# Kernel optimization log

Hardware: AMD Instinct MI355X
Metric: run time of the kernel (lower is better)

## Reference

```python
import jax, jax.numpy as jnp
import numpy as np

S, D, H = 2048, 2048, 16
HD = D // H  # head dim = 128
LN_EPS = 1e-5


def _ln(x, g, b):
    mu = jnp.mean(x, axis=-1, keepdims=True)
    var = jnp.var(x, axis=-1, keepdims=True)
    return (x - mu) / jnp.sqrt(var + LN_EPS) * g + b


def setup_inputs() -> dict:
    key = jax.random.key(0)
    ks = jax.random.split(key, 8)
    B = 2
    s = 0.02  # weight init scale
    return {
        "x": jax.random.normal(ks[0], (B, S, D), jnp.float32),
        "Wq": jax.random.normal(ks[1], (D, D), jnp.float32) * s,
        "bq": jnp.zeros((D,), jnp.float32),
        "Wk": jax.random.normal(ks[2], (D, D), jnp.float32) * s,
        "bk": jnp.zeros((D,), jnp.float32),
        "Wv": jax.random.normal(ks[3], (D, D), jnp.float32) * s,
        "bv": jnp.zeros((D,), jnp.float32),
        "Wo": jax.random.normal(ks[4], (D, D), jnp.float32) * s,
        "bo": jnp.zeros((D,), jnp.float32),
        "ln1_g": jnp.ones((D,), jnp.float32),
        "ln1_b": jnp.zeros((D,), jnp.float32),
        "ln2_g": jnp.ones((D,), jnp.float32),
        "ln2_b": jnp.zeros((D,), jnp.float32),
        "W1": jax.random.normal(ks[5], (4 * D, D), jnp.float32) * s,
        "b1": jnp.zeros((4 * D,), jnp.float32),
        "W2": jax.random.normal(ks[6], (D, 4 * D), jnp.float32) * s,
        "b2": jnp.zeros((D,), jnp.float32),
    }


def reference(x, Wq, bq, Wk, bk, Wv, bv, Wo, bo,
              ln1_g, ln1_b, ln2_g, ln2_b, W1, b1, W2, b2):
    causal = jnp.tril(jnp.ones((S, S), bool))  # [S, S] lower-triangular mask
    neg = jnp.finfo(x.dtype).min
    inv_sqrt_hd = 1.0 / jnp.sqrt(jnp.asarray(HD, x.dtype))

    def block(xs):  # xs: [S, D] (equinox module is per-sequence; vmapped over batch)
        h = _ln(xs, ln1_g, ln1_b)
        q = (h @ Wq.T + bq).reshape(S, H, HD)
        k = (h @ Wk.T + bk).reshape(S, H, HD)
        v = (h @ Wv.T + bv).reshape(S, H, HD)
        logits = jnp.einsum('shd,Shd->hsS', q, k) * inv_sqrt_hd
        logits = jnp.where(causal, logits, neg)
        attn = jax.nn.softmax(logits, axis=-1)
        o = jnp.einsum('hsS,Shd->shd', attn, v).reshape(S, D)
        h = h + (o @ Wo.T + bo)          # residual of post-ln1 value (as in source)
        h2 = _ln(h, ln2_g, ln2_b)
        m = jax.nn.gelu(h2 @ W1.T + b1) @ W2.T + b2
        return h2 + m                    # residual of post-ln2 value (as in source)

    return jax.vmap(block)(x)
```

## Files before the change

kernel.cpp:

```cpp
#include <hip/hip_runtime.h>
#include <hip/hip_bf16.h>
#include <math.h>

#define DD   2048
#define SS   2048
#define HH   16
#define HDIM 128
#define BB   2
#define MM   4096
#define D4   8192

using bf16x8 = __attribute__((ext_vector_type(8))) short;
using f32x4  = __attribute__((ext_vector_type(4))) float;
using f32x16 = __attribute__((ext_vector_type(16))) float;

__device__ __forceinline__ ushort f2bf(float x) {
  uint u = __builtin_bit_cast(uint, x);
  u += 0x7FFFu + ((u >> 16) & 1u);
  return (ushort)(u >> 16);
}
__device__ __forceinline__ float bf2f(ushort u) {
  return __builtin_bit_cast(float, (uint)u << 16);
}
__device__ __forceinline__ uint pkbf2(float a, float b) {
  return (uint)f2bf(a) | ((uint)f2bf(b) << 16);
}

__device__ __forceinline__ float gelu_f(float v) {
  float u = 0.7978845608028654f * (v + 0.044715f * v * v * v);
  float e = __expf(2.0f * u);
  float th = 1.0f - 2.0f / (e + 1.0f);
  return 0.5f * v * (1.0f + th);
}

__device__ __forceinline__ void gload_lds16(const void* g, void* l) {
  __builtin_amdgcn_global_load_lds(
      (const __attribute__((address_space(1))) void*)g,
      (__attribute__((address_space(3))) void*)l, 16, 0, 0);
}

__global__ __launch_bounds__(256) void cvt_f32_bf16(
    const float* __restrict__ in, ushort* __restrict__ out, int n4) {
  int i = blockIdx.x * 256 + threadIdx.x;
  if (i >= n4) return;
  float4 v = ((const float4*)in)[i];
  ushort4 o;
  o.x = f2bf(v.x); o.y = f2bf(v.y); o.z = f2bf(v.z); o.w = f2bf(v.w);
  ((ushort4*)out)[i] = o;
}

__global__ __launch_bounds__(256) void ln_rows(
    const float* __restrict__ in, const float* __restrict__ gam,
    const float* __restrict__ bet, ushort* __restrict__ outb) {
  int row = blockIdx.x;
  int t = threadIdx.x;
  const float4* r4 = (const float4*)(in + (size_t)row * DD);
  float4 v0 = r4[t], v1 = r4[t + 256];
  float s = v0.x + v0.y + v0.z + v0.w + v1.x + v1.y + v1.z + v1.w;
  __shared__ float redA[4], redB[4];
  #pragma unroll
  for (int off = 32; off >= 1; off >>= 1) s += __shfl_xor(s, off);
  if ((t & 63) == 0) redA[t >> 6] = s;
  __syncthreads();
  float mean = (redA[0] + redA[1] + redA[2] + redA[3]) * (1.0f / DD);
  float d0 = v0.x - mean, d1 = v0.y - mean, d2 = v0.z - mean, d3 = v0.w - mean;
  float d4 = v1.x - mean, d5 = v1.y - mean, d6 = v1.z - mean, d7 = v1.w - mean;
  float q = d0*d0 + d1*d1 + d2*d2 + d3*d3 + d4*d4 + d5*d5 + d6*d6 + d7*d7;
  #pragma unroll
  for (int off = 32; off >= 1; off >>= 1) q += __shfl_xor(q, off);
  if ((t & 63) == 0) redB[t >> 6] = q;
  __syncthreads();
  float var = (redB[0] + redB[1] + redB[2] + redB[3]) * (1.0f / DD);
  float rstd = rsqrtf(var + 1e-5f);
  const float4* g4 = (const float4*)gam;
  const float4* b4 = (const float4*)bet;
  float4 g0 = g4[t], g1 = g4[t + 256], bb0 = b4[t], bb1 = b4[t + 256];
  float4 y0, y1;
  y0.x = d0 * rstd * g0.x + bb0.x;  y0.y = d1 * rstd * g0.y + bb0.y;
  y0.z = d2 * rstd * g0.z + bb0.z;  y0.w = d3 * rstd * g0.w + bb0.w;
  y1.x = d4 * rstd * g1.x + bb1.x;  y1.y = d5 * rstd * g1.y + bb1.y;
  y1.z = d6 * rstd * g1.z + bb1.z;  y1.w = d7 * rstd * g1.w + bb1.w;
  ushort4 u0, u1;
  u0.x = f2bf(y0.x); u0.y = f2bf(y0.y); u0.z = f2bf(y0.z); u0.w = f2bf(y0.w);
  u1.x = f2bf(y1.x); u1.y = f2bf(y1.y); u1.z = f2bf(y1.z); u1.w = f2bf(y1.w);
  ushort4* ob4 = (ushort4*)(outb + (size_t)row * DD);
  ob4[t] = u0; ob4[t + 256] = u1;
}

template <int OMODE, bool GELU_, bool RES_>
__global__ __launch_bounds__(512, 2) void gemm2(
    const ushort* __restrict__ A, const ushort* __restrict__ Bt,
    const float* __restrict__ pb0, const float* __restrict__ pb1,
    const float* __restrict__ pb2, const ushort* __restrict__ res,
    void* __restrict__ Cout, int M, int N, int K) {
  extern __shared__ __align__(16) ushort smem[];
  const int nbm = M >> 8, nbn = N >> 7;
  const int nwg = nbm * nbn;
  int wg = blockIdx.x;
  int wg2 = (wg & 7) * (nwg >> 3) + (wg >> 3);
  int bm = wg2 % nbm, bn = wg2 / nbm;
  int m0 = bm << 8, n0 = bn << 7;
  int t = threadIdx.x, lane = t & 63, w = t >> 6;
  int wm = w >> 2, wn = w & 3;
  int lr = lane & 15, lg = lane >> 4;

  auto stage = [&](int kt, int slot) {
    int k0 = kt << 6;
    ushort* lA = smem + slot * 24576;
    ushort* lB = lA + 16384;
    #pragma unroll
    for (int r = 0; r < 4; r++) {
      int idx = (r << 9) + t;
      int row = idx >> 3, ch = idx & 7;
      gload_lds16(A + (size_t)(m0 + row) * K + k0 + ((ch ^ (row & 7)) << 3),
                  lA + idx * 8);
    }
    #pragma unroll
    for (int r = 0; r < 2; r++) {
      int idx = (r << 9) + t;
      int row = idx >> 3, ch = idx & 7;
      gload_lds16(Bt + (size_t)(n0 + row) * K + k0 + ((ch ^ (row & 7)) << 3),
                  lB + idx * 8);
    }
  };

  f32x4 acc[8][2] = {};
  const int NT = K >> 6;
  stage(0, 0);
  stage(1, 1);
  int slot = 0;
  for (int kt = 0; kt < NT; ++kt) {
    __builtin_amdgcn_sched_barrier(0);
    if (kt + 1 < NT)
      asm volatile("s_waitcnt vmcnt(6) lgkmcnt(0)" ::: "memory");
    else
      asm volatile("s_waitcnt vmcnt(0) lgkmcnt(0)" ::: "memory");
    __builtin_amdgcn_s_barrier();
    __builtin_amdgcn_sched_barrier(0);
    if (kt + 2 < NT) {
      int s2 = slot + 2; if (s2 >= 3) s2 -= 3;
      stage(kt + 2, s2);
    }
    const ushort* lA = smem + slot * 24576;
    const ushort* lB = lA + 16384;
    bf16x8 af[8][2], bfr[2][2];
    #pragma unroll
    for (int mi = 0; mi < 8; mi++) {
      int row = wm * 128 + mi * 16 + lr;
      #pragma unroll
      for (int ks = 0; ks < 2; ks++)
        af[mi][ks] = *(const bf16x8*)
            &lA[row * 64 + (((ks * 4 + lg) ^ (row & 7)) << 3)];
    }
    #pragma unroll
    for (int ni = 0; ni < 2; ni++) {
      int row = wn * 32 + ni * 16 + lr;
      #pragma unroll
      for (int ks = 0; ks < 2; ks++)
        bfr[ni][ks] = *(const bf16x8*)
            &lB[row * 64 + (((ks * 4 + lg) ^ (row & 7)) << 3)];
    }
    __builtin_amdgcn_s_setprio(1);
    #pragma unroll
    for (int ks = 0; ks < 2; ks++)
      #pragma unroll
      for (int mi = 0; mi < 8; mi++)
        #pragma unroll
        for (int ni = 0; ni < 2; ni++)
          acc[mi][ni] = __builtin_amdgcn_mfma_f32_16x16x32_bf16(
              af[mi][ks], bfr[ni][ks], acc[mi][ni], 0, 0, 0);
    __builtin_amdgcn_s_setprio(0);
    slot = (slot + 1 == 3) ? 0 : slot + 1;
  }

  if (OMODE == 3) {
    int seg = n0 >> 11;
    const float* pb = (seg == 0) ? pb0 : (seg == 1) ? pb1 : pb2;
    int c0 = n0 & 2047;
    float bv[2];
    #pragma unroll
    for (int ni = 0; ni < 2; ni++) bv[ni] = pb[c0 + wn * 32 + ni * 16 + lr];
    if (seg < 2) {
      ushort* q_or_k = (ushort*)Cout + (size_t)seg * MM * DD;
      #pragma unroll
      for (int mi = 0; mi < 8; mi++) {
        #pragma unroll
        for (int r = 0; r < 4; r++) {
          int m = m0 + wm * 128 + mi * 16 + lg * 4 + r;
          #pragma unroll
          for (int ni = 0; ni < 2; ni++) {
            int col = c0 + wn * 32 + ni * 16 + lr;
            q_or_k[(size_t)m * DD + col] = f2bf(acc[mi][ni][r] + bv[ni]);
          }
        }
      }
    } else {
      ushort* vT = (ushort*)Cout + (size_t)2 * MM * DD;
      #pragma unroll
      for (int mi = 0; mi < 8; mi++) {
        int mg = m0 + wm * 128 + mi * 16 + lg * 4;
        int bb_ = mg >> 11, sb = mg & 2047;
        #pragma unroll
        for (int ni = 0; ni < 2; ni++) {
          int col = c0 + wn * 32 + ni * 16 + lr;
          int h = col >> 7, d = col & 127;
          ushort4 u4;
          u4.x = f2bf(acc[mi][ni][0] + bv[ni]);
          u4.y = f2bf(acc[mi][ni][1] + bv[ni]);
          u4.z = f2bf(acc[mi][ni][2] + bv[ni]);
          u4.w = f2bf(acc[mi][ni][3] + bv[ni]);
          size_t idx = ((size_t)(bb_ * 16 + h) * 128 + d) * 2048 + sb;
          *(ushort4*)&vT[idx] = u4;
        }
      }
    }
    return;
  }

  float bv[2];
  #pragma unroll
  for (int ni = 0; ni < 2; ni++) bv[ni] = pb0[n0 + wn * 32 + ni * 16 + lr];
  #pragma unroll
  for (int mi = 0; mi < 8; mi++) {
    #pragma unroll
    for (int r = 0; r < 4; r++) {
      int m = m0 + wm * 128 + mi * 16 + lg * 4 + r;
      #pragma unroll
      for (int ni = 0; ni < 2; ni++) {
        int n = n0 + wn * 32 + ni * 16 + lr;
        size_t idx = (size_t)m * N + n;
        float v = acc[mi][ni][r] + bv[ni];
        if (RES_) v += bf2f(res[idx]);
        if (GELU_) v = gelu_f(v);
        if (OMODE == 1) ((ushort*)Cout)[idx] = f2bf(v);
        else            ((float*)Cout)[idx] = v;
      }
    }
  }
}

__global__ __launch_bounds__(256) void attn_fwd(
    const ushort* __restrict__ qb, const ushort* __restrict__ kb,
    const ushort* __restrict__ vTb, ushort* __restrict__ ob) {
  extern __shared__ __align__(16) ushort asm_[];
  ushort* KsB = asm_;
  ushort* VsB = asm_ + 16384;
  ushort* Pw  = asm_ + 32768 + (threadIdx.x >> 6) * 2048;

  int blk = blockIdx.x;
  int i15 = blk & 15;
  int qt = (blk & 256) ? i15 : 15 - i15;
  int bh = blk >> 4;
  int b = bh >> 4, h = bh & 15;
  int q0 = qt << 7;
  int t = threadIdx.x, lane = t & 63, w = t >> 6;
  int l31 = lane & 31, hi = lane >> 5;
  const size_t base = (size_t)b * SS * DD + (size_t)h * HDIM;
  const ushort* qp = qb + base;
  const ushort* kp = kb + base;
  const ushort* vp = vTb + (size_t)bh * HDIM * SS;
  int wq0 = q0 + w * 32;
  int qg = wq0 + l31;

  bf16x8 qf[8];
  #pragma unroll
  for (int kk = 0; kk < 8; kk++)
    qf[kk] = *(const bf16x8*)(qp + (size_t)qg * DD + kk * 16 + hi * 8);

  auto stageKV = [&](int it, int buf) {
    int kv0 = it * 64;
    ushort* Kd = KsB + buf * 8192;
    ushort* Vd = VsB + buf * 8192;
    #pragma unroll
    for (int ii = 0; ii < 4; ii++) {
      int chunk = ii * 256 + t;
      int row = chunk >> 4, cc = chunk & 15;
      gload_lds16(kp + (size_t)(kv0 + row) * DD + ((cc ^ (row & 15)) << 3),
                  Kd + chunk * 8);
    }
    #pragma unroll
    for (int ii = 0; ii < 4; ii++) {
      int chunk = ii * 256 + t;
      int row = chunk >> 3, cc = chunk & 7;
      gload_lds16(vp + (size_t)row * SS + kv0 + ((cc ^ (row & 7)) << 3),
                  Vd + chunk * 8);
    }
  };

  f32x16 o[4] = {};
  float mu = -1e30f, lrow = 0.f;
  const float csc = 0.08838834764831845f * 1.4426950408889634f;

  int nIter = 2 * qt + 2;
  stageKV(0, 0);
  asm volatile("s_waitcnt vmcnt(0)" ::: "memory");
  __builtin_amdgcn_s_barrier();
  int cur = 0;
  for (int it = 0; it < nIter; ++it) {
    int kv0 = it * 64;
    if (it + 1 < nIter) stageKV(it + 1, cur ^ 1);

    if (kv0 <= wq0 + 31) {
      const ushort* Kc = KsB + cur * 8192;
      const ushort* Vc = VsB + cur * 8192;
      f32x16 s2[2] = {};
      #pragma unroll
      for (int nt = 0; nt < 2; nt++) {
        int row = nt * 32 + l31;
        #pragma unroll
        for (int kk = 0; kk < 8; kk++) {
          bf16x8 kf = *(const bf16x8*)
              &Kc[row * 128 + (((kk * 2 + hi) ^ (row & 15)) << 3)];
          s2[nt] = __builtin_amdgcn_mfma_f32_32x32x16_bf16(kf, qf[kk], s2[nt],
                                                           0, 0, 0);
        }
      }
      bool full = (kv0 + 63 <= wq0);
      float pm[4] = {-3e38f, -3e38f, -3e38f, -3e38f};
      if (full) {
        #pragma unroll
        for (int nt = 0; nt < 2; nt++)
          #pragma unroll
          for (int g2 = 0; g2 < 4; g2++)
            #pragma unroll
            for (int i = 0; i < 4; i++) {
              float u = s2[nt][g2 * 4 + i] * csc;
              s2[nt][g2 * 4 + i] = u;
              pm[i] = fmaxf(pm[i], u);
            }
      } else {
        #pragma unroll
        for (int nt = 0; nt < 2; nt++)
          #pragma unroll
          for (int g2 = 0; g2 < 4; g2++)
            #pragma unroll
            for (int i = 0; i < 4; i++) {
              int kvl = nt * 32 + g2 * 8 + 4 * hi + i;
              float u = (kv0 + kvl > qg) ? -3e38f : s2[nt][g2 * 4 + i] * csc;
              s2[nt][g2 * 4 + i] = u;
              pm[i] = fmaxf(pm[i], u);
            }
      }
      float mx = fmaxf(fmaxf(pm[0], pm[1]), fmaxf(pm[2], pm[3]));
      mx = fmaxf(mx, __shfl_xor(mx, 32));
      if (!__all(mx - mu <= 8.0f)) {
        float mnew = fmaxf(mu, mx);
        float fr = exp2f(mu - mnew);
        mu = mnew;
        lrow *= fr;
        #pragma unroll
        for (int dt = 0; dt < 4; dt++)
          #pragma unroll
          for (int r = 0; r < 16; r++) o[dt][r] *= fr;
      }
      float ps[4] = {0.f, 0.f, 0.f, 0.f};
      #pragma unroll
      for (int nt = 0; nt < 2; nt++)
        #pragma unroll
        for (int g2 = 0; g2 < 4; g2++)
          #pragma unroll
          for (int i = 0; i < 4; i++) {
            float p = exp2f(s2[nt][g2 * 4 + i] - mu);
            s2[nt][g2 * 4 + i] = p;
            ps[i] += p;
          }
      float sum = (ps[0] + ps[1]) + (ps[2] + ps[3]);
      sum += __shfl_xor(sum, 32);
      lrow += sum;
      #pragma unroll
      for (int nt = 0; nt < 2; nt++) {
        #pragma unroll
        for (int g2 = 0; g2 < 4; g2++) {
          uint2 u;
          u.x = pkbf2(s2[nt][g2 * 4 + 0], s2[nt][g2 * 4 + 1]);
          u.y = pkbf2(s2[nt][g2 * 4 + 2], s2[nt][g2 * 4 + 3]);
          int cp = (nt * 4 + g2) ^ (l31 & 7);
          *(uint2*)&Pw[l31 * 64 + cp * 8 + hi * 4] = u;
        }
      }
      asm volatile("s_waitcnt lgkmcnt(0)" ::: "memory");
      #pragma unroll
      for (int kk = 0; kk < 4; kk++) {
        bf16x8 pf = *(const bf16x8*)
            &Pw[l31 * 64 + (((kk * 2 + hi) ^ (l31 & 7)) << 3)];
        #pragma unroll
        for (int dt = 0; dt < 4; dt++) {
          int drow = dt * 32 + l31;
          bf16x8 vf = *(const bf16x8*)
              &Vc[drow * 64 + (((kk * 2 + hi) ^ (drow & 7)) << 3)];
          o[dt] = __builtin_amdgcn_mfma_f32_32x32x16_bf16(vf, pf, o[dt],
                                                          0, 0, 0);
        }
      }
    }
    asm volatile("s_waitcnt vmcnt(0)" ::: "memory");
    __builtin_amdgcn_s_barrier();
    cur ^= 1;
  }

  float inv = 1.0f / lrow;
  #pragma unroll
  for (int dt = 0; dt < 4; dt++) {
    #pragma unroll
    for (int g2 = 0; g2 < 4; g2++) {
      uint2 u;
      u.x = pkbf2(o[dt][g2 * 4 + 0] * inv, o[dt][g2 * 4 + 1] * inv);
      u.y = pkbf2(o[dt][g2 * 4 + 2] * inv, o[dt][g2 * 4 + 3] * inv);
      int d = dt * 32 + 8 * g2 + 4 * hi;
      *(uint2*)&ob[base + (size_t)qg * DD + d] = u;
    }
  }
}

extern "C" void kernel_launch(void* const* d_in, const int* in_sizes, int n_in,
                              void* d_out, int out_size, void* d_ws,
                              size_t ws_size, hipStream_t stream) {
  const float* x    = (const float*)d_in[0];
  const float* Wq   = (const float*)d_in[1];
  const float* bq   = (const float*)d_in[2];
  const float* Wk   = (const float*)d_in[3];
  const float* bk   = (const float*)d_in[4];
  const float* Wv   = (const float*)d_in[5];
  const float* bv   = (const float*)d_in[6];
  const float* Wo   = (const float*)d_in[7];
  const float* bo   = (const float*)d_in[8];
  const float* ln1g = (const float*)d_in[9];
  const float* ln1b = (const float*)d_in[10];
  const float* ln2g = (const float*)d_in[11];
  const float* ln2b = (const float*)d_in[12];
  const float* W1   = (const float*)d_in[13];
  const float* b1   = (const float*)d_in[14];
  const float* W2   = (const float*)d_in[15];
  const float* b2   = (const float*)d_in[16];

  char* ws = (char*)d_ws;
  ushort* Wqkvb = (ushort*)(ws);
  ushort* Wob   = Wqkvb + (size_t)3 * DD * DD;
  ushort* W1b = (ushort*)(ws);
  ushort* W2b = W1b + (size_t)D4 * DD;
  ushort* qkvb = (ushort*)(ws + 67108864);
  ushort* qbf = qkvb;
  ushort* kbf = qbf + (size_t)MM * DD;
  ushort* vTt = kbf + (size_t)MM * DD;
  ushort* aob = vTt + (size_t)MM * DD;
  ushort* gb  = (ushort*)(ws + 67108864);
  ushort* hb  = (ushort*)(ws + 167772160);
  ushort* h2b = hb;
  float* h2in = (float*)(ws + 184549376);
  float* out  = (float*)d_out;

  const int LDSB = 147456;
  const int LDSA = 81920;
  (void)hipFuncSetAttribute((const void*)gemm2<3, false, false>,
                      hipFuncAttributeMaxDynamicSharedMemorySize, LDSB);
  (void)hipFuncSetAttribute((const void*)gemm2<0, false, true>,
                      hipFuncAttributeMaxDynamicSharedMemorySize, LDSB);
  (void)hipFuncSetAttribute((const void*)gemm2<1, true, false>,
                      hipFuncAttributeMaxDynamicSharedMemorySize, LDSB);
  (void)hipFuncSetAttribute((const void*)attn_fwd,
                      hipFuncAttributeMaxDynamicSharedMemorySize, LDSA);

  dim3 blk(256);
  dim3 gblk(512);
  cvt_f32_bf16<<<DD * DD / 1024, blk, 0, stream>>>(Wq, Wqkvb, DD * DD / 4);
  cvt_f32_bf16<<<DD * DD / 1024, blk, 0, stream>>>(Wk, Wqkvb + (size_t)DD * DD, DD * DD / 4);
  cvt_f32_bf16<<<DD * DD / 1024, blk, 0, stream>>>(Wv, Wqkvb + (size_t)2 * DD * DD, DD * DD / 4);
  cvt_f32_bf16<<<DD * DD / 1024, blk, 0, stream>>>(Wo, Wob, DD * DD / 4);
  ln_rows<<<MM, blk, 0, stream>>>(x, ln1g, ln1b, hb);
  gemm2<3, false, false><<<768, gblk, LDSB, stream>>>(
      hb, Wqkvb, bq, bk, bv, nullptr, qkvb, MM, 3 * DD, DD);
  attn_fwd<<<512, blk, LDSA, stream>>>(qbf, kbf, vTt, aob);
  gemm2<0, false, true><<<256, gblk, LDSB, stream>>>(
      aob, Wob, bo, bo, bo, hb, h2in, MM, DD, DD);
  ln_rows<<<MM, blk, 0, stream>>>(h2in, ln2g, ln2b, h2b);
  cvt_f32_bf16<<<D4 * DD / 1024, blk, 0, stream>>>(W1, W1b, D4 * DD / 4);
  cvt_f32_bf16<<<D4 * DD / 1024, blk, 0, stream>>>(W2, W2b, D4 * DD / 4);
  gemm2<1, true, false><<<1024, gblk, LDSB, stream>>>(
      h2b, W1b, b1, b1, b1, nullptr, gb, MM, D4, DD);
  gemm2<0, false, true><<<256, gblk, LDSB, stream>>>(
      gb, W2b, b2, b2, b2, h2b, out, MM, DD, D4);
}
```

Before: 628.7 us.

## Add 256x256 quadrant-pipelined GEMM kernel and split-K for MLP down projection

Adds a new GEMM kernel with 256x256 tiles, double-buffered direct global-to-LDS loads, and a quadrant-by-quadrant MFMA schedule that overlaps the next k-tile's loads with compute. It replaces the QKV and MLP-up GEMMs. The W2 GEMM becomes split-K over two halves writing bf16 partials, and a new elementwise kernel sums them with the bias and residual. This should raise per-tile data reuse and fill the GPU better on the K=8192 GEMM. The cost is an extra partial-sum pass over memory and bf16 rounding of the partials.

```diff
diff --git a/kernel.cpp b/kernel.cpp
--- a/kernel.cpp
+++ b/kernel.cpp
@@ -90,8 +90,7 @@
 template <int OMODE, bool GELU_, bool RES_>
 __global__ __launch_bounds__(512, 2) void gemm2(
     const ushort* __restrict__ A, const ushort* __restrict__ Bt,
-    const float* __restrict__ pb0, const float* __restrict__ pb1,
-    const float* __restrict__ pb2, const ushort* __restrict__ res,
+    const float* __restrict__ pb0, const ushort* __restrict__ res,
     void* __restrict__ Cout, int M, int N, int K) {
   extern __shared__ __align__(16) ushort smem[];
   const int nbm = M >> 8, nbn = N >> 7;
@@ -173,13 +172,191 @@
     slot = (slot + 1 == 3) ? 0 : slot + 1;
   }
 
-  if (OMODE == 3) {
+  float bv[2];
+  #pragma unroll
+  for (int ni = 0; ni < 2; ni++) bv[ni] = pb0[n0 + wn * 32 + ni * 16 + lr];
+  #pragma unroll
+  for (int mi = 0; mi < 8; mi++) {
+    #pragma unroll
+    for (int r = 0; r < 4; r++) {
+      int m = m0 + wm * 128 + mi * 16 + lg * 4 + r;
+      #pragma unroll
+      for (int ni = 0; ni < 2; ni++) {
+        int n = n0 + wn * 32 + ni * 16 + lr;
+        size_t idx = (size_t)m * N + n;
+        float v = acc[mi][ni][r] + bv[ni];
+        if (RES_) v += bf2f(res[idx]);
+        if (GELU_) v = gelu_f(v);
+        if (OMODE == 1) ((ushort*)Cout)[idx] = f2bf(v);
+        else            ((float*)Cout)[idx] = v;
+      }
+    }
+  }
+}
+
+#define MF16(MQ, NQ, BARR) \
+  { _Pragma("unroll") for (int ks = 0; ks < 2; ks++) { \
+    _Pragma("unroll") for (int fm = 0; fm < 4; fm++) { \
+      _Pragma("unroll") for (int fn = 0; fn < 2; fn++) { \
+        acc[MQ * 4 + fm][NQ * 2 + fn] = \
+            __builtin_amdgcn_mfma_f32_16x16x32_bf16( \
+                aR[fm][ks], BARR[fn][ks], acc[MQ * 4 + fm][NQ * 2 + fn], \
+                0, 0, 0); } } } }
+
+template <int OMODE, bool GELU_>
+__global__ __launch_bounds__(512, 2) void gemm8(
+    const ushort* __restrict__ A, const ushort* __restrict__ Bt,
+    const float* __restrict__ pb0, const float* __restrict__ pb1,
+    const float* __restrict__ pb2,
+    void* __restrict__ Cout, int M, int N, int Kfull, int Kloc) {
+  extern __shared__ __align__(16) ushort smem[];
+  const int nbm = M >> 8, nbn = N >> 8;
+  const int nwg = nbm * nbn;
+  int wgr = blockIdx.x;
+  int ksl = 0;
+  if (OMODE == 4) { ksl = wgr / nwg; wgr -= ksl * nwg; }
+  int wg2 = (wgr & 7) * (nwg >> 3) + (wgr >> 3);
+  int bm = wg2 % nbm, bn = wg2 / nbm;
+  int m0 = bm << 8, n0 = bn << 8;
+  size_t kbase = (size_t)ksl * Kloc;
+  int t = threadIdx.x, lane = t & 63, w = t >> 6;
+  int wm = w >> 2, wn = w & 3;
+  int lr = lane & 15, lg = lane >> 4;
+
+  int srow = t >> 3;
+  int ssw = ((t & 7) ^ (srow & 7)) << 3;
+  const ushort* pA1 = A + (size_t)(m0 + srow) * Kfull + kbase + ssw;
+  const ushort* pB1 = Bt +
+      (size_t)(n0 + (srow >> 5) * 64 + (srow & 31)) * Kfull + kbase + ssw;
+  const size_t K32 = (size_t)32 * Kfull, K64 = (size_t)64 * Kfull,
+               K128 = (size_t)128 * Kfull;
+  ushort* dA = smem + t * 8;
+  ushort* dB = smem + 16384 + t * 8;
+
+  auto stage = [&](int kt, int h) {
+    int boff = (kt & 1) << 15;
+    size_t ko = (size_t)kt << 6;
+    if (h < 2) {
+      const ushort* g = pA1 + (size_t)h * K64 + ko;
+      ushort* d = dA + boff + h * 8192;
+      gload_lds16(g, d);
+      gload_lds16(g + K128, d + 4096);
+    } else {
+      const ushort* g = pB1 + (size_t)(h - 2) * K32 + ko;
+      ushort* d = dB + boff + (h - 2) * 8192;
+      gload_lds16(g, d);
+      gload_lds16(g + K128, d + 4096);
+    }
+  };
+
+  int swz0 = (lg ^ (lr & 7)) << 3;
+  int swz1 = ((4 + lg) ^ (lr & 7)) << 3;
+  int arb[4], brb[2];
+  #pragma unroll
+  for (int f = 0; f < 4; f++) arb[f] = (wm * 64 + f * 16 + lr) * 64;
+  #pragma unroll
+  for (int f = 0; f < 2; f++) brb[f] = (wn * 32 + f * 16 + lr) * 64;
+
+  f32x4 acc[8][4] = {};
+  bf16x8 aR[4][2], bR0[2][2], bR1[2][2];
+  const int NT = Kloc >> 6;
+
+  stage(0, 0); stage(0, 1); stage(0, 2); stage(0, 3);
+  asm volatile("s_waitcnt vmcnt(0)" ::: "memory");
+  __builtin_amdgcn_s_barrier();
+
+  for (int kt = 0; kt < NT; ++kt) {
+    const ushort* hA = smem + ((kt & 1) << 15);
+    const ushort* hB = hA + 16384;
+    bool st = (kt + 1 < NT);
+    #pragma unroll
+    for (int f = 0; f < 4; f++) {
+      aR[f][0] = *(const bf16x8*)&hA[arb[f] + swz0];
+      aR[f][1] = *(const bf16x8*)&hA[arb[f] + swz1];
+    }
+    #pragma unroll
+    for (int f = 0; f < 2; f++) {
+      bR0[f][0] = *(const bf16x8*)&hB[brb[f] + swz0];
+      bR0[f][1] = *(const bf16x8*)&hB[brb[f] + swz1];
+    }
+    if (st) stage(kt + 1, 0);
+    asm volatile("s_waitcnt lgkmcnt(8)" ::: "memory");
+    __builtin_amdgcn_sched_barrier(0);
+    __builtin_amdgcn_s_barrier();
+    asm volatile("s_waitcnt lgkmcnt(0)" ::: "memory");
+    __builtin_amdgcn_sched_barrier(0);
+    __builtin_amdgcn_s_setprio(1);
+    MF16(0, 0, bR0);
+    __builtin_amdgcn_s_setprio(0);
+    __builtin_amdgcn_sched_barrier(0);
+    if (st) { asm volatile("s_waitcnt vmcnt(4)" ::: "memory"); }
+    else    { asm volatile("s_waitcnt vmcnt(2)" ::: "memory"); }
+    __builtin_amdgcn_s_barrier();
+    #pragma unroll
+    for (int f = 0; f < 2; f++) {
+      bR1[f][0] = *(const bf16x8*)&hB[8192 + brb[f] + swz0];
+      bR1[f][1] = *(const bf16x8*)&hB[8192 + brb[f] + swz1];
+    }
+    if (st) stage(kt + 1, 2);
+    __builtin_amdgcn_sched_barrier(0);
+    __builtin_amdgcn_s_barrier();
+    asm volatile("s_waitcnt lgkmcnt(0)" ::: "memory");
+    __builtin_amdgcn_sched_barrier(0);
+    __builtin_amdgcn_s_setprio(1);
+    MF16(0, 1, bR1);
+    __builtin_amdgcn_s_setprio(0);
+    __builtin_amdgcn_sched_barrier(0);
+    if (st) { asm volatile("s_waitcnt vmcnt(4)" ::: "memory"); }
+    else    { asm volatile("s_waitcnt vmcnt(0)" ::: "memory"); }
+    __builtin_amdgcn_s_barrier();
+    #pragma unroll
+    for (int f = 0; f < 4; f++) {
+      aR[f][0] = *(const bf16x8*)&hA[8192 + arb[f] + swz0];
+      aR[f][1] = *(const bf16x8*)&hA[8192 + arb[f] + swz1];
+    }
+    if (st) stage(kt + 1, 3);
+    __builtin_amdgcn_sched_barrier(0);
+    __builtin_amdgcn_s_barrier();
+    asm volatile("s_waitcnt lgkmcnt(0)" ::: "memory");
+    __builtin_amdgcn_sched_barrier(0);
+    __builtin_amdgcn_s_setprio(1);
+    MF16(1, 1, bR1);
+    __builtin_amdgcn_s_setprio(0);
+    __builtin_amdgcn_sched_barrier(0);
+    __builtin_amdgcn_s_barrier();
+    if (st) stage(kt + 1, 1);
+    __builtin_amdgcn_sched_barrier(0);
+    __builtin_amdgcn_s_barrier();
+    __builtin_amdgcn_sched_barrier(0);
+    __builtin_amdgcn_s_setprio(1);
+    MF16(1, 0, bR0);
+    __builtin_amdgcn_s_setprio(0);
+    __builtin_amdgcn_sched_barrier(0);
+    if (st) { asm volatile("s_waitcnt vmcnt(4)" ::: "memory"); }
+    __builtin_amdgcn_s_barrier();
+  }
+
+  if constexpr (OMODE == 4) {
+    ushort* Cp = (ushort*)Cout + (size_t)ksl * M * N;
+    #pragma unroll
+    for (int mi = 0; mi < 8; mi++) {
+      #pragma unroll
+      for (int r = 0; r < 4; r++) {
+        int m = m0 + wm * 128 + mi * 16 + lg * 4 + r;
+        #pragma unroll
+        for (int ni = 0; ni < 4; ni++) {
+          int n = n0 + wn * 64 + ni * 16 + lr;
+          Cp[(size_t)m * N + n] = f2bf(acc[mi][ni][r]);
+        }
+      }
+    }
+  } else if constexpr (OMODE == 3) {
     int seg = n0 >> 11;
     const float* pb = (seg == 0) ? pb0 : (seg == 1) ? pb1 : pb2;
     int c0 = n0 & 2047;
-    float bv[2];
-    #pragma unroll
-    for (int ni = 0; ni < 2; ni++) bv[ni] = pb[c0 + wn * 32 + ni * 16 + lr];
+    float bv[4];
+    #pragma unroll
+    for (int ni = 0; ni < 4; ni++) bv[ni] = pb[c0 + wn * 64 + ni * 16 + lr];
     if (seg < 2) {
       ushort* q_or_k = (ushort*)Cout + (size_t)seg * MM * DD;
       #pragma unroll
@@ -188,8 +365,8 @@
         for (int r = 0; r < 4; r++) {
           int m = m0 + wm * 128 + mi * 16 + lg * 4 + r;
           #pragma unroll
-          for (int ni = 0; ni < 2; ni++) {
-            int col = c0 + wn * 32 + ni * 16 + lr;
+          for (int ni = 0; ni < 4; ni++) {
+            int col = c0 + wn * 64 + ni * 16 + lr;
             q_or_k[(size_t)m * DD + col] = f2bf(acc[mi][ni][r] + bv[ni]);
           }
         }
@@ -201,8 +378,8 @@
         int mg = m0 + wm * 128 + mi * 16 + lg * 4;
         int bb_ = mg >> 11, sb = mg & 2047;
         #pragma unroll
-        for (int ni = 0; ni < 2; ni++) {
-          int col = c0 + wn * 32 + ni * 16 + lr;
+        for (int ni = 0; ni < 4; ni++) {
+          int col = c0 + wn * 64 + ni * 16 + lr;
           int h = col >> 7, d = col & 127;
           ushort4 u4;
           u4.x = f2bf(acc[mi][ni][0] + bv[ni]);
@@ -214,29 +391,41 @@
         }
       }
     }
-    return;
+  } else {
+    float bv[4];
+    #pragma unroll
+    for (int ni = 0; ni < 4; ni++) bv[ni] = pb0[n0 + wn * 64 + ni * 16 + lr];
+    #pragma unroll
+    for (int mi = 0; mi < 8; mi++) {
+      #pragma unroll
+      for (int r = 0; r < 4; r++) {
+        int m = m0 + wm * 128 + mi * 16 + lg * 4 + r;
+        #pragma unroll
+        for (int ni = 0; ni < 4; ni++) {
+          int n = n0 + wn * 64 + ni * 16 + lr;
+          float v = acc[mi][ni][r] + bv[ni];
+          if (GELU_) v = gelu_f(v);
+          ((ushort*)Cout)[(size_t)m * N + n] = f2bf(v);
+        }
+      }
+    }
   }
-
-  float bv[2];
-  #pragma unroll
-  for (int ni = 0; ni < 2; ni++) bv[ni] = pb0[n0 + wn * 32 + ni * 16 + lr];
-  #pragma unroll
-  for (int mi = 0; mi < 8; mi++) {
-    #pragma unroll
-    for (int r = 0; r < 4; r++) {
-      int m = m0 + wm * 128 + mi * 16 + lg * 4 + r;
-      #pragma unroll
-      for (int ni = 0; ni < 2; ni++) {
-        int n = n0 + wn * 32 + ni * 16 + lr;
-        size_t idx = (size_t)m * N + n;
-        float v = acc[mi][ni][r] + bv[ni];
-        if (RES_) v += bf2f(res[idx]);
-        if (GELU_) v = gelu_f(v);
-        if (OMODE == 1) ((ushort*)Cout)[idx] = f2bf(v);
-        else            ((float*)Cout)[idx] = v;
-      }
-    }
-  }
+}
+
+__global__ __launch_bounds__(256) void mlp_fin(
+    const ushort* __restrict__ p, const ushort* __restrict__ res,
+    const float* __restrict__ bias, float* __restrict__ out) {
+  int i4 = blockIdx.x * 256 + threadIdx.x;
+  ushort4 a = ((const ushort4*)p)[i4];
+  ushort4 b = ((const ushort4*)(p + (size_t)MM * DD))[i4];
+  ushort4 r = ((const ushort4*)res)[i4];
+  float4 g = ((const float4*)bias)[i4 & 511];
+  float4 o;
+  o.x = bf2f(a.x) + bf2f(b.x) + bf2f(r.x) + g.x;
+  o.y = bf2f(a.y) + bf2f(b.y) + bf2f(r.y) + g.y;
+  o.z = bf2f(a.z) + bf2f(b.z) + bf2f(r.z) + g.z;
+  o.w = bf2f(a.w) + bf2f(b.w) + bf2f(r.w) + g.w;
+  ((float4*)out)[i4] = o;
 }
 
 __global__ __launch_bounds__(256) void attn_fwd(
@@ -447,16 +636,20 @@
   ushort* hb  = (ushort*)(ws + 167772160);
   ushort* h2b = hb;
   float* h2in = (float*)(ws + 184549376);
+  ushort* pD  = (ushort*)(ws + 184549376);
   float* out  = (float*)d_out;
 
   const int LDSB = 147456;
+  const int LDSC = 131072;
   const int LDSA = 81920;
-  (void)hipFuncSetAttribute((const void*)gemm2<3, false, false>,
-                      hipFuncAttributeMaxDynamicSharedMemorySize, LDSB);
   (void)hipFuncSetAttribute((const void*)gemm2<0, false, true>,
                       hipFuncAttributeMaxDynamicSharedMemorySize, LDSB);
-  (void)hipFuncSetAttribute((const void*)gemm2<1, true, false>,
-                      hipFuncAttributeMaxDynamicSharedMemorySize, LDSB);
+  (void)hipFuncSetAttribute((const void*)gemm8<3, false>,
+                      hipFuncAttributeMaxDynamicSharedMemorySize, LDSC);
+  (void)hipFuncSetAttribute((const void*)gemm8<1, true>,
+                      hipFuncAttributeMaxDynamicSharedMemorySize, LDSC);
+  (void)hipFuncSetAttribute((const void*)gemm8<4, false>,
+                      hipFuncAttributeMaxDynamicSharedMemorySize, LDSC);
   (void)hipFuncSetAttribute((const void*)attn_fwd,
                       hipFuncAttributeMaxDynamicSharedMemorySize, LDSA);
 
@@ -467,16 +660,17 @@
   cvt_f32_bf16<<<DD * DD / 1024, blk, 0, stream>>>(Wv, Wqkvb + (size_t)2 * DD * DD, DD * DD / 4);
   cvt_f32_bf16<<<DD * DD / 1024, blk, 0, stream>>>(Wo, Wob, DD * DD / 4);
   ln_rows<<<MM, blk, 0, stream>>>(x, ln1g, ln1b, hb);
-  gemm2<3, false, false><<<768, gblk, LDSB, stream>>>(
-      hb, Wqkvb, bq, bk, bv, nullptr, qkvb, MM, 3 * DD, DD);
+  gemm8<3, false><<<384, gblk, LDSC, stream>>>(
+      hb, Wqkvb, bq, bk, bv, qkvb, MM, 3 * DD, DD, DD);
   attn_fwd<<<512, blk, LDSA, stream>>>(qbf, kbf, vTt, aob);
   gemm2<0, false, true><<<256, gblk, LDSB, stream>>>(
-      aob, Wob, bo, bo, bo, hb, h2in, MM, DD, DD);
+      aob, Wob, bo, hb, h2in, MM, DD, DD);
   ln_rows<<<MM, blk, 0, stream>>>(h2in, ln2g, ln2b, h2b);
   cvt_f32_bf16<<<D4 * DD / 1024, blk, 0, stream>>>(W1, W1b, D4 * DD / 4);
   cvt_f32_bf16<<<D4 * DD / 1024, blk, 0, stream>>>(W2, W2b, D4 * DD / 4);
-  gemm2<1, true, false><<<1024, gblk, LDSB, stream>>>(
-      h2b, W1b, b1, b1, b1, nullptr, gb, MM, D4, DD);
-  gemm2<0, false, true><<<256, gblk, LDSB, stream>>>(
-      gb, W2b, b2, b2, b2, h2b, out, MM, DD, D4);
-}
+  gemm8<1, true><<<512, gblk, LDSC, stream>>>(
+      h2b, W1b, b1, b1, b1, gb, MM, D4, DD, DD);
+  gemm8<4, false><<<256, gblk, LDSC, stream>>>(
+      gb, W2b, b2, b2, b2, pD, MM, DD, D4, D4 / 2);
+  mlp_fin<<<MM * DD / 1024, blk, 0, stream>>>(pD, h2b, b2, out);
+}
```

Result: no change. 637.9 us (+1.5%).
